# Performance work log

Measured on AMD Instinct MI355X. Metric: run time of the kernel, lower is better.

## Reference

```python
import jax, jax.numpy as jnp
import numpy as np

TOP_K = 2
POOL = 4  # EfficientSpatialRouter.pool_scale


def silu(v):
    return v * jax.nn.sigmoid(v)


def setup_inputs() -> dict:
    key = jax.random.key(0)
    ks = jax.random.split(key, 6)
    B, C, H, W = 16, 256, 56, 56
    E, O = 4, 256
    hidden = 2 * C            # SimpleExpert expand_ratio=2
    red = max(C // 8, 8)      # router reduced_channels
    x = jax.random.normal(ks[0], (B, C, H, W), jnp.float32)
    router_w1 = jax.random.normal(ks[1], (red, C, 3, 3), jnp.float32) * 0.02
    router_w2 = jax.random.normal(ks[2], (E, red), jnp.float32) * 0.01
    expert_w1 = jax.random.normal(ks[3], (E, hidden, C), jnp.float32) * 0.05
    expert_w2 = jax.random.normal(ks[4], (E, O, hidden), jnp.float32) * 0.03
    shared_w = jax.random.normal(ks[5], (O, C), jnp.float32) * 0.05
    return {"x": x, "router_w1": router_w1, "router_w2": router_w2,
            "expert_w1": expert_w1, "expert_w2": expert_w2, "shared_w": shared_w}


def reference(x, router_w1, router_w2, expert_w1, expert_w2, shared_w):
    # Eval mode: no router noise; BatchNorm with default running stats
    # (mean=0, var=1, gamma=1, beta=0) is the identity, so BNs are omitted.
    B, C, H, W = x.shape
    E = router_w2.shape[0]

    # --- EfficientSpatialRouter ---
    xp = x.reshape(B, C, H // POOL, POOL, W // POOL, POOL).mean(axis=(3, 5))
    h = jax.lax.conv_general_dilated(
        xp, router_w1, window_strides=(1, 1), padding=((1, 1), (1, 1)),
        dimension_numbers=("NCHW", "OIHW", "NCHW"))
    h = silu(h)  # [B, red, H/4, W/4]
    # 1x1 conv to E channels then spatial mean == mean of per-pixel logits
    logits = jnp.einsum("er,brij->be", router_w2, h) / (h.shape[2] * h.shape[3])
    probs = jax.nn.softmax(logits, axis=1)
    topv, topi = jax.lax.top_k(probs, TOP_K)          # [B,k]
    topv = topv / (topv.sum(axis=1, keepdims=True) + 1e-6)

    # --- shared expert (1x1 conv + BN(id) + SiLU) ---
    shared = silu(jnp.einsum("oc,bcij->boij", shared_w, x))

    # --- all SimpleExperts densely (1x1 conv -> SiLU -> 1x1 conv) ---
    hid = silu(jnp.einsum("edc,bcij->bedij", expert_w1, x))   # [B,E,hid,H,W]
    eo = jnp.einsum("eod,bedij->beoij", expert_w2, hid)       # [B,E,O,H,W]

    # --- weighted combine of top-k experts ---
    wdense = jnp.zeros((B, E), x.dtype).at[jnp.arange(B)[:, None], topi].add(topv)
    expert_out = jnp.einsum("be,beoij->boij", wdense, eo)
    return shared + expert_out
```

## Files before the change

### kernel.cpp

```cpp
#include <hip/hip_runtime.h>
#include <hip/hip_bf16.h>

typedef __attribute__((ext_vector_type(8))) short bf16x8;
typedef __attribute__((ext_vector_type(16))) float f32x16;
typedef __attribute__((ext_vector_type(4))) unsigned short ushort4v;

static __device__ __forceinline__ unsigned short f2bf(float f) {
  unsigned u = __float_as_uint(f);
  return (unsigned short)((u + 0x7FFFu + ((u >> 16) & 1u)) >> 16);
}
static __device__ __forceinline__ float silu_f(float v) { return v / (1.f + __expf(-v)); }

__global__ void prep_k(const float* __restrict__ shw, const float* __restrict__ ew1,
                       const float* __restrict__ ew2, const float* __restrict__ x,
                       unsigned short* __restrict__ wshp, unsigned short* __restrict__ w1p,
                       unsigned short* __restrict__ w2p, float* __restrict__ xp) {
  const int bid = blockIdx.x;
  if (bid < 4352) {
    int idx = bid * 256 + threadIdx.x;
    if (idx < 65536) {
      int j = idx;
      int i = j & 7, l = (j >> 3) & 63, ks = (j >> 9) & 15, rb = j >> 13;
      int row = rb * 32 + (l & 31), k = ks * 16 + (l >> 5) * 8 + i;
      wshp[j] = f2bf(shw[row * 256 + k]);
    } else if (idx < 589824) {
      int j = idx - 65536;
      int i = j & 7, l = (j >> 3) & 63, ks = (j >> 9) & 15, rb = (j >> 13) & 15, e = j >> 17;
      int row = rb * 32 + (l & 31), k = ks * 16 + (l >> 5) * 8 + i;
      w1p[j] = f2bf(ew1[((size_t)e * 512 + row) * 256 + k]);
    } else if (idx < 1114112) {
      int j = idx - 589824;
      int i = j & 7, l = (j >> 3) & 63, ks = (j >> 9) & 31, rb = (j >> 14) & 7, e = j >> 17;
      int row = rb * 32 + (l & 31), k = ks * 16 + (l >> 5) * 8 + i;
      w2p[j] = f2bf(ew2[((size_t)e * 256 + row) * 512 + k]);
    }
  } else {
    int idx = (bid - 4352) * 256 + threadIdx.x;
    if (idx >= 16 * 256 * 196) return;
    int pj = idx % 14, tmp = idx / 14, pi = tmp % 14, bc = tmp / 14;
    const float* src = x + (size_t)bc * 3136 + pi * 4 * 56 + pj * 4;
    float s = 0.f;
#pragma unroll
    for (int u = 0; u < 4; ++u) {
      float4 v = *reinterpret_cast<const float4*>(src + u * 56);
      s += v.x + v.y + v.z + v.w;
    }
    xp[idx] = s * 0.0625f;
  }
}

__global__ __launch_bounds__(256) void router_conv_k(const float* __restrict__ xp,
                                                     const float* __restrict__ rw1,
                                                     float* __restrict__ hsum) {
  const int b = blockIdx.x >> 5, r = blockIdx.x & 31;
  __shared__ float wl[2304];
  __shared__ float xl[32][256];
  __shared__ float red[4];
  const int t = threadIdx.x;
  for (int i = t; i < 2304; i += 256) wl[i] = rw1[r * 2304 + i];
  for (int i = t; i < 32 * 256; i += 256) (&xl[0][0])[i] = 0.f;
  const int pi = t / 14, pj = t % 14;
  float acc = 0.f;
  for (int cc = 0; cc < 8; ++cc) {
    __syncthreads();
    for (int i = t; i < 32 * 196; i += 256) {
      int c = i / 196, px = i % 196;
      xl[c][(px / 14 + 1) * 16 + (px % 14 + 1)] =
          xp[((size_t)b * 256 + cc * 32 + c) * 196 + px];
    }
    __syncthreads();
    if (t < 196) {
      for (int c = 0; c < 32; ++c) {
        const float* wp = &wl[(cc * 32 + c) * 9];
        const float* xc = &xl[c][pi * 16 + pj];
#pragma unroll
        for (int u = 0; u < 3; ++u)
#pragma unroll
          for (int v = 0; v < 3; ++v) acc += xc[u * 16 + v] * wp[u * 3 + v];
      }
    }
  }
  float s = (t < 196) ? silu_f(acc) : 0.f;
#pragma unroll
  for (int off = 32; off > 0; off >>= 1) s += __shfl_down(s, off);
  if ((t & 63) == 0) red[t >> 6] = s;
  __syncthreads();
  if (t == 0) hsum[b * 32 + r] = red[0] + red[1] + red[2] + red[3];
}

__global__ void topk_k(const float* __restrict__ hsum, const float* __restrict__ rw2,
                       float* __restrict__ selv, int* __restrict__ sele) {
  const int t = threadIdx.x;
  const int b = t >> 2, e = t & 3;
  float l = 0.f;
#pragma unroll
  for (int r = 0; r < 32; ++r) l += rw2[e * 32 + r] * hsum[b * 32 + r];
  l *= (1.f / 196.f);
  float m = fmaxf(l, __shfl_xor(l, 1));
  m = fmaxf(m, __shfl_xor(m, 2));
  float p = __expf(l - m);
  float sm = p + __shfl_xor(p, 1);
  sm += __shfl_xor(sm, 2);
  float prob = p / sm;
  float p0 = __shfl(prob, (b << 2) | 0);
  float p1 = __shfl(prob, (b << 2) | 1);
  float p2 = __shfl(prob, (b << 2) | 2);
  float p3 = __shfl(prob, (b << 2) | 3);
  if (e == 0) {
    float pr[4] = {p0, p1, p2, p3};
    int i1 = 0;
    for (int i = 1; i < 4; ++i)
      if (pr[i] > pr[i1]) i1 = i;
    int i2 = (i1 == 0) ? 1 : 0;
    for (int i = 0; i < 4; ++i) {
      if (i == i1 || i == i2) continue;
      if (pr[i] > pr[i2]) i2 = i;
    }
    float denom = pr[i1] + pr[i2] + 1e-6f;
    selv[b * 2 + 0] = pr[i1] / denom;
    selv[b * 2 + 1] = pr[i2] / denom;
    sele[b * 2 + 0] = i1;
    sele[b * 2 + 1] = i2;
  }
}

static __device__ __forceinline__ void gemm_k256(
    const unsigned short* __restrict__ A0, const unsigned short* __restrict__ A1,
    const unsigned short* B0, const unsigned short* B1, f32x16 acc[2][2]) {
  bf16x8 aA[2], bA[2], aB[2], bB[2];
  aA[0] = *reinterpret_cast<const bf16x8*>(A0);
  aA[1] = *reinterpret_cast<const bf16x8*>(A1);
  bA[0] = *reinterpret_cast<const bf16x8*>(B0);
  bA[1] = *reinterpret_cast<const bf16x8*>(B1);
#pragma unroll
  for (int kk = 0; kk < 16; kk += 2) {
    aB[0] = *reinterpret_cast<const bf16x8*>(A0 + (kk + 1) * 512);
    aB[1] = *reinterpret_cast<const bf16x8*>(A1 + (kk + 1) * 512);
    bB[0] = *reinterpret_cast<const bf16x8*>(B0 + (kk + 1) * 1024);
    bB[1] = *reinterpret_cast<const bf16x8*>(B1 + (kk + 1) * 1024);
    acc[0][0] = __builtin_amdgcn_mfma_f32_32x32x16_bf16(aA[0], bA[0], acc[0][0], 0, 0, 0);
    acc[0][1] = __builtin_amdgcn_mfma_f32_32x32x16_bf16(aA[0], bA[1], acc[0][1], 0, 0, 0);
    acc[1][0] = __builtin_amdgcn_mfma_f32_32x32x16_bf16(aA[1], bA[0], acc[1][0], 0, 0, 0);
    acc[1][1] = __builtin_amdgcn_mfma_f32_32x32x16_bf16(aA[1], bA[1], acc[1][1], 0, 0, 0);
    if (kk + 2 < 16) {
      aA[0] = *reinterpret_cast<const bf16x8*>(A0 + (kk + 2) * 512);
      aA[1] = *reinterpret_cast<const bf16x8*>(A1 + (kk + 2) * 512);
      bA[0] = *reinterpret_cast<const bf16x8*>(B0 + (kk + 2) * 1024);
      bA[1] = *reinterpret_cast<const bf16x8*>(B1 + (kk + 2) * 1024);
    }
    acc[0][0] = __builtin_amdgcn_mfma_f32_32x32x16_bf16(aB[0], bB[0], acc[0][0], 0, 0, 0);
    acc[0][1] = __builtin_amdgcn_mfma_f32_32x32x16_bf16(aB[0], bB[1], acc[0][1], 0, 0, 0);
    acc[1][0] = __builtin_amdgcn_mfma_f32_32x32x16_bf16(aB[1], bB[0], acc[1][0], 0, 0, 0);
    acc[1][1] = __builtin_amdgcn_mfma_f32_32x32x16_bf16(aB[1], bB[1], acc[1][1], 0, 0, 0);
  }
}

__global__ __launch_bounds__(256, 2) void moe_main_k(
    const float* __restrict__ x, const unsigned short* __restrict__ wshp,
    const unsigned short* __restrict__ w1p, const unsigned short* __restrict__ w2p,
    const float* __restrict__ selv, const int* __restrict__ sele,
    float* __restrict__ out) {
  constexpr int HW = 3136;
  __shared__ __align__(16) unsigned short xs[32 * 64 * 8];
  __shared__ __align__(16) unsigned short hs[32 * 64 * 8];

  const int b = blockIdx.x / 49, tile = blockIdx.x - b * 49;
  const int px0 = tile * 64;
  const int t = threadIdx.x;
  const int w = t >> 6, l = t & 63;
  const int l31 = l & 31, lh = l >> 5;

  {
    const float* xb = x + (size_t)b * 256 * HW + px0 + l;
#pragma unroll
    for (int cg = 0; cg < 8; ++cg) {
      const int c0 = w * 64 + cg * 8;
      alignas(16) unsigned short tmp[8];
#pragma unroll
      for (int i = 0; i < 8; ++i) tmp[i] = f2bf(xb[(size_t)(c0 + i) * HW]);
      *reinterpret_cast<bf16x8*>(&xs[((c0 >> 3) * 64 + l) * 8]) =
          *reinterpret_cast<const bf16x8*>(tmp);
    }
  }

  const unsigned short* xB0 = xs + (lh * 64 + l31) * 8;
  const unsigned short* xB1 = xB0 + 32 * 8;
  const unsigned short* hB0 = hs + (lh * 64 + l31) * 8;
  const unsigned short* hB1 = hB0 + 32 * 8;

  f32x16 oacc[2][2];
#pragma unroll
  for (int i = 0; i < 2; ++i)
#pragma unroll
    for (int j = 0; j < 2; ++j)
#pragma unroll
      for (int r = 0; r < 16; ++r) oacc[i][j][r] = 0.f;

  __syncthreads();

  {
    const unsigned short* A0 = wshp + (size_t)(w * 2) * 16 * 512 + l * 8;
    gemm_k256(A0, A0 + 8192, xB0, xB1, oacc);
  }
#pragma unroll
  for (int i = 0; i < 2; ++i)
#pragma unroll
    for (int j = 0; j < 2; ++j)
#pragma unroll
      for (int r = 0; r < 16; ++r) oacc[i][j][r] = silu_f(oacc[i][j][r]);

#pragma unroll 1
  for (int ei = 0; ei < 2; ++ei) {
    const int e = sele[b * 2 + ei];
    const float v = selv[b * 2 + ei];
#pragma unroll 1
    for (int ph = 0; ph < 2; ++ph) {
      f32x16 hacc[2][2];
#pragma unroll
      for (int i = 0; i < 2; ++i)
#pragma unroll
        for (int j = 0; j < 2; ++j)
#pragma unroll
          for (int r = 0; r < 16; ++r) hacc[i][j][r] = 0.f;
      {
        const unsigned short* A0 =
            w1p + (size_t)(e * 16 + ph * 8 + w * 2) * 16 * 512 + l * 8;
        gemm_k256(A0, A0 + 8192, xB0, xB1, hacc);
      }
      __syncthreads();
#pragma unroll
      for (int rfi = 0; rfi < 2; ++rfi)
#pragma unroll
        for (int cf = 0; cf < 2; ++cf) {
#pragma unroll
          for (int g = 0; g < 4; ++g) {
            alignas(8) unsigned short pk[4];
#pragma unroll
            for (int j = 0; j < 4; ++j)
              pk[j] = f2bf(v * silu_f(hacc[rfi][cf][g * 4 + j]));
            const int kg = w * 8 + rfi * 4 + g;
            const int ui = (kg * 64 + cf * 32 + l31) * 8 + lh * 4;
            *reinterpret_cast<ushort4v*>(&hs[ui]) = *reinterpret_cast<const ushort4v*>(pk);
          }
        }
      __syncthreads();
      {
        const unsigned short* A0 =
            w2p + ((size_t)(e * 8 + w * 2) * 32 + ph * 16) * 512 + l * 8;
        gemm_k256(A0, A0 + 16384, hB0, hB1, oacc);
      }
    }
  }

#pragma unroll
  for (int rfi = 0; rfi < 2; ++rfi)
#pragma unroll
    for (int cf = 0; cf < 2; ++cf)
#pragma unroll
      for (int r = 0; r < 16; ++r) {
        const int o = w * 64 + rfi * 32 + (r & 3) + 8 * (r >> 2) + 4 * lh;
        out[((size_t)b * 256 + o) * HW + px0 + cf * 32 + l31] = oacc[rfi][cf][r];
      }
}

extern "C" void kernel_launch(void* const* d_in, const int* in_sizes, int n_in,
                              void* d_out, int out_size, void* d_ws, size_t ws_size,
                              hipStream_t stream) {
  const float* x = (const float*)d_in[0];
  const float* rw1 = (const float*)d_in[1];
  const float* rw2 = (const float*)d_in[2];
  const float* ew1 = (const float*)d_in[3];
  const float* ew2 = (const float*)d_in[4];
  const float* shw = (const float*)d_in[5];
  float* out = (float*)d_out;
  char* ws = (char*)d_ws;

  float* xp = (float*)(ws);
  float* hsum = (float*)(ws + 3211264);
  float* selv = (float*)(ws + 3213312);
  int* sele = (int*)(ws + 3213440);
  unsigned short* wshp = (unsigned short*)(ws + 3213568);
  unsigned short* w1p = wshp + 65536;
  unsigned short* w2p = w1p + 524288;

  prep_k<<<7488, 256, 0, stream>>>(shw, ew1, ew2, x, wshp, w1p, w2p, xp);
  router_conv_k<<<512, 256, 0, stream>>>(xp, rw1, hsum);
  topk_k<<<1, 64, 0, stream>>>(hsum, rw2, selv, sele);
  moe_main_k<<<784, 256, 0, stream>>>(x, wshp, w1p, w2p, selv, sele, out);
}
```

Measured before the change: 168.8 us.

## Split expert hidden dim into four chunks to cut registers and LDS for occupancy 3

The expert hidden dimension is now processed in four chunks of 128 instead of two of 256. The first GEMM uses a single row fragment per wave, which halves the hidden accumulator registers and the hs shared buffer, and launch bounds are raised to allow three blocks per CU. The aim is more waves in flight to hide load latency. The cost is twice as many barrier pairs per expert and shorter K loops in the second GEMM, each with its own prologue.

Result: slower. 181.3 us (+7.4%).

```diff
diff --git a/kernel.cpp b/kernel.cpp
--- a/kernel.cpp
+++ b/kernel.cpp
@@ -124,7 +124,8 @@
   }
 }
 
-static __device__ __forceinline__ void gemm_k256(
+template <int NKS>
+static __device__ __forceinline__ void gemm_rf2(
     const unsigned short* __restrict__ A0, const unsigned short* __restrict__ A1,
     const unsigned short* B0, const unsigned short* B1, f32x16 acc[2][2]) {
   bf16x8 aA[2], bA[2], aB[2], bB[2];
@@ -133,7 +134,7 @@
   bA[0] = *reinterpret_cast<const bf16x8*>(B0);
   bA[1] = *reinterpret_cast<const bf16x8*>(B1);
 #pragma unroll
-  for (int kk = 0; kk < 16; kk += 2) {
+  for (int kk = 0; kk < NKS; kk += 2) {
     aB[0] = *reinterpret_cast<const bf16x8*>(A0 + (kk + 1) * 512);
     aB[1] = *reinterpret_cast<const bf16x8*>(A1 + (kk + 1) * 512);
     bB[0] = *reinterpret_cast<const bf16x8*>(B0 + (kk + 1) * 1024);
@@ -142,7 +143,7 @@
     acc[0][1] = __builtin_amdgcn_mfma_f32_32x32x16_bf16(aA[0], bA[1], acc[0][1], 0, 0, 0);
     acc[1][0] = __builtin_amdgcn_mfma_f32_32x32x16_bf16(aA[1], bA[0], acc[1][0], 0, 0, 0);
     acc[1][1] = __builtin_amdgcn_mfma_f32_32x32x16_bf16(aA[1], bA[1], acc[1][1], 0, 0, 0);
-    if (kk + 2 < 16) {
+    if (kk + 2 < NKS) {
       aA[0] = *reinterpret_cast<const bf16x8*>(A0 + (kk + 2) * 512);
       aA[1] = *reinterpret_cast<const bf16x8*>(A1 + (kk + 2) * 512);
       bA[0] = *reinterpret_cast<const bf16x8*>(B0 + (kk + 2) * 1024);
@@ -155,14 +156,38 @@
   }
 }
 
-__global__ __launch_bounds__(256, 2) void moe_main_k(
+static __device__ __forceinline__ void gemm_rf1_k256(
+    const unsigned short* __restrict__ A0, const unsigned short* B0,
+    const unsigned short* B1, f32x16 acc[2]) {
+  bf16x8 aA, bA[2], aB, bB[2];
+  aA = *reinterpret_cast<const bf16x8*>(A0);
+  bA[0] = *reinterpret_cast<const bf16x8*>(B0);
+  bA[1] = *reinterpret_cast<const bf16x8*>(B1);
+#pragma unroll
+  for (int kk = 0; kk < 16; kk += 2) {
+    aB = *reinterpret_cast<const bf16x8*>(A0 + (kk + 1) * 512);
+    bB[0] = *reinterpret_cast<const bf16x8*>(B0 + (kk + 1) * 1024);
+    bB[1] = *reinterpret_cast<const bf16x8*>(B1 + (kk + 1) * 1024);
+    acc[0] = __builtin_amdgcn_mfma_f32_32x32x16_bf16(aA, bA[0], acc[0], 0, 0, 0);
+    acc[1] = __builtin_amdgcn_mfma_f32_32x32x16_bf16(aA, bA[1], acc[1], 0, 0, 0);
+    if (kk + 2 < 16) {
+      aA = *reinterpret_cast<const bf16x8*>(A0 + (kk + 2) * 512);
+      bA[0] = *reinterpret_cast<const bf16x8*>(B0 + (kk + 2) * 1024);
+      bA[1] = *reinterpret_cast<const bf16x8*>(B1 + (kk + 2) * 1024);
+    }
+    acc[0] = __builtin_amdgcn_mfma_f32_32x32x16_bf16(aB, bB[0], acc[0], 0, 0, 0);
+    acc[1] = __builtin_amdgcn_mfma_f32_32x32x16_bf16(aB, bB[1], acc[1], 0, 0, 0);
+  }
+}
+
+__global__ __launch_bounds__(256, 3) void moe_main_k(
     const float* __restrict__ x, const unsigned short* __restrict__ wshp,
     const unsigned short* __restrict__ w1p, const unsigned short* __restrict__ w2p,
     const float* __restrict__ selv, const int* __restrict__ sele,
     float* __restrict__ out) {
   constexpr int HW = 3136;
   __shared__ __align__(16) unsigned short xs[32 * 64 * 8];
-  __shared__ __align__(16) unsigned short hs[32 * 64 * 8];
+  __shared__ __align__(16) unsigned short hs[16 * 64 * 8];
 
   const int b = blockIdx.x / 49, tile = blockIdx.x - b * 49;
   const int px0 = tile * 64;
@@ -200,7 +225,7 @@
 
   {
     const unsigned short* A0 = wshp + (size_t)(w * 2) * 16 * 512 + l * 8;
-    gemm_k256(A0, A0 + 8192, xB0, xB1, oacc);
+    gemm_rf2<16>(A0, A0 + 8192, xB0, xB1, oacc);
   }
 #pragma unroll
   for (int i = 0; i < 2; ++i)
@@ -214,40 +239,35 @@
     const int e = sele[b * 2 + ei];
     const float v = selv[b * 2 + ei];
 #pragma unroll 1
-    for (int ph = 0; ph < 2; ++ph) {
-      f32x16 hacc[2][2];
-#pragma unroll
-      for (int i = 0; i < 2; ++i)
-#pragma unroll
-        for (int j = 0; j < 2; ++j)
-#pragma unroll
-          for (int r = 0; r < 16; ++r) hacc[i][j][r] = 0.f;
+    for (int ch = 0; ch < 4; ++ch) {
+      f32x16 hacc[2];
+#pragma unroll
+      for (int cf = 0; cf < 2; ++cf)
+#pragma unroll
+        for (int r = 0; r < 16; ++r) hacc[cf][r] = 0.f;
       {
         const unsigned short* A0 =
-            w1p + (size_t)(e * 16 + ph * 8 + w * 2) * 16 * 512 + l * 8;
-        gemm_k256(A0, A0 + 8192, xB0, xB1, hacc);
+            w1p + (size_t)(e * 16 + ch * 4 + w) * 16 * 512 + l * 8;
+        gemm_rf1_k256(A0, xB0, xB1, hacc);
       }
       __syncthreads();
 #pragma unroll
-      for (int rfi = 0; rfi < 2; ++rfi)
-#pragma unroll
-        for (int cf = 0; cf < 2; ++cf) {
-#pragma unroll
-          for (int g = 0; g < 4; ++g) {
-            alignas(8) unsigned short pk[4];
-#pragma unroll
-            for (int j = 0; j < 4; ++j)
-              pk[j] = f2bf(v * silu_f(hacc[rfi][cf][g * 4 + j]));
-            const int kg = w * 8 + rfi * 4 + g;
-            const int ui = (kg * 64 + cf * 32 + l31) * 8 + lh * 4;
-            *reinterpret_cast<ushort4v*>(&hs[ui]) = *reinterpret_cast<const ushort4v*>(pk);
-          }
+      for (int cf = 0; cf < 2; ++cf) {
+#pragma unroll
+        for (int g = 0; g < 4; ++g) {
+          alignas(8) unsigned short pk[4];
+#pragma unroll
+          for (int j = 0; j < 4; ++j) pk[j] = f2bf(v * silu_f(hacc[cf][g * 4 + j]));
+          const int kg = w * 4 + g;
+          const int ui = (kg * 64 + cf * 32 + l31) * 8 + lh * 4;
+          *reinterpret_cast<ushort4v*>(&hs[ui]) = *reinterpret_cast<const ushort4v*>(pk);
         }
+      }
       __syncthreads();
       {
         const unsigned short* A0 =
-            w2p + ((size_t)(e * 8 + w * 2) * 32 + ph * 16) * 512 + l * 8;
-        gemm_k256(A0, A0 + 16384, hB0, hB1, oacc);
+            w2p + ((size_t)(e * 8 + w * 2) * 32 + ch * 8) * 512 + l * 8;
+        gemm_rf2<8>(A0, A0 + 16384, hB0, hB1, oacc);
       }
     }
   }
```
